# Optimization experiments

Hardware: AMD Instinct MI355X
Metric: run time of the kernel (lower is better)

Reference implementation:

```python
import jax, jax.numpy as jnp
import numpy as np
from jax import lax

B, CIN, H, W = 2, 512, 64, 64
NCLS = 5
CI = CIN // 4      # inter_channels = 128
CQ = CI // 8       # PAM query/key channels = 16
EPS = 1e-5


def setup_inputs() -> dict:
    key = jax.random.key(0)
    it = iter(jax.random.split(key, 48))

    def nrm(shape, s=0.05):
        return jax.random.normal(next(it), shape, jnp.float32) * s

    def bn(c):
        w = jax.random.uniform(next(it), (c,), jnp.float32, 0.5, 1.5)
        b = nrm((c,))
        m = nrm((c,))
        v = jax.random.uniform(next(it), (c,), jnp.float32, 0.5, 1.5)
        return w, b, m, v

    inp = {}
    inp['x'] = jax.random.normal(next(it), (B, CIN, H, W), jnp.float32)
    inp['bn_a_w'], inp['bn_a_b'], inp['bn_a_m'], inp['bn_a_v'] = bn(CIN)
    inp['conv_a_w'] = nrm((CI, CIN, 3, 3))
    inp['bn_c_w'], inp['bn_c_b'], inp['bn_c_m'], inp['bn_c_v'] = bn(CIN)
    inp['conv_c_w'] = nrm((CI, CIN, 3, 3))
    inp['pam_q_w'] = nrm((CQ, CI)); inp['pam_q_b'] = nrm((CQ,))
    inp['pam_k_w'] = nrm((CQ, CI)); inp['pam_k_b'] = nrm((CQ,))
    inp['pam_v_w'] = nrm((CI, CI)); inp['pam_v_b'] = nrm((CI,))
    inp['pam_gamma'] = nrm((1,), 0.5)
    inp['cam_gamma'] = nrm((1,), 0.5)
    inp['bn_a1_w'], inp['bn_a1_b'], inp['bn_a1_m'], inp['bn_a1_v'] = bn(CI)
    inp['conv_a1_w'] = nrm((CIN, CI)); inp['conv_a1_b'] = nrm((CIN,))
    inp['bn_c1_w'], inp['bn_c1_b'], inp['bn_c1_m'], inp['bn_c1_v'] = bn(CI)
    inp['conv_c1_w'] = nrm((CIN, CI)); inp['conv_c1_b'] = nrm((CIN,))
    inp['out_a_w'] = nrm((NCLS, CIN)); inp['out_a_b'] = nrm((NCLS,))
    inp['out_c_w'] = nrm((NCLS, CIN)); inp['out_c_b'] = nrm((NCLS,))
    inp['out_f_w'] = nrm((NCLS, CIN)); inp['out_f_b'] = nrm((NCLS,))
    return inp


def _bn_relu(x, w, b, m, v):
    # eval-mode BatchNorm2d followed by ReLU
    scale = (w / jnp.sqrt(v + EPS))[None, :, None, None]
    shift = (b - m * w / jnp.sqrt(v + EPS))[None, :, None, None]
    return jax.nn.relu(x * scale + shift)


def _conv3(x, w):
    return lax.conv_general_dilated(x, w, (1, 1), 'SAME',
                                    dimension_numbers=('NCHW', 'OIHW', 'NCHW'))


def _conv1(x, w, b):
    # 1x1 conv as channel matmul
    return jnp.einsum('oi,bihw->bohw', w, x) + b[None, :, None, None]


def _pam(x, wq, bq, wk, bk, wv, bv, gamma):
    Bc, C, Hh, Ww = x.shape
    N = Hh * Ww
    q = _conv1(x, wq, bq).reshape(Bc, -1, N)   # [B,CQ,N]
    k = _conv1(x, wk, bk).reshape(Bc, -1, N)   # [B,CQ,N]
    v = _conv1(x, wv, bv).reshape(Bc, C, N)    # [B,C,N]
    energy = jnp.einsum('bcn,bcm->bnm', q, k)  # [B,N,N]
    attn = jax.nn.softmax(energy, axis=-1)
    out = jnp.einsum('bcm,bnm->bcn', v, attn).reshape(Bc, C, Hh, Ww)
    return gamma * out + x


def _cam(x, gamma):
    Bc, C, Hh, Ww = x.shape
    N = Hh * Ww
    f = x.reshape(Bc, C, N)
    energy = jnp.einsum('bcn,bdn->bcd', f, f)                    # [B,C,C]
    energy_new = jnp.max(energy, -1, keepdims=True) - energy
    attn = jax.nn.softmax(energy_new, axis=-1)
    out = jnp.einsum('bcd,bdn->bcn', attn, f).reshape(Bc, C, Hh, Ww)
    return gamma * out + x


def reference(x, bn_a_w, bn_a_b, bn_a_m, bn_a_v, conv_a_w,
              bn_c_w, bn_c_b, bn_c_m, bn_c_v, conv_c_w,
              pam_q_w, pam_q_b, pam_k_w, pam_k_b, pam_v_w, pam_v_b,
              pam_gamma, cam_gamma,
              bn_a1_w, bn_a1_b, bn_a1_m, bn_a1_v, conv_a1_w, conv_a1_b,
              bn_c1_w, bn_c1_b, bn_c1_m, bn_c1_v, conv_c1_w, conv_c1_b,
              out_a_w, out_a_b, out_c_w, out_c_b, out_f_w, out_f_b):
    # position-attention branch
    sa = _conv3(_bn_relu(x, bn_a_w, bn_a_b, bn_a_m, bn_a_v), conv_a_w)
    sa = _pam(sa, pam_q_w, pam_q_b, pam_k_w, pam_k_b, pam_v_w, pam_v_b, pam_gamma)
    sa = _conv1(_bn_relu(sa, bn_a1_w, bn_a1_b, bn_a1_m, bn_a1_v), conv_a1_w, conv_a1_b)
    # channel-attention branch
    sc = _conv3(_bn_relu(x, bn_c_w, bn_c_b, bn_c_m, bn_c_v), conv_c_w)
    sc = _cam(sc, cam_gamma)
    sc = _conv1(_bn_relu(sc, bn_c1_w, bn_c1_b, bn_c1_m, bn_c1_v), conv_c1_w, conv_c1_b)
    feat_fusion = sa + sc
    # dropout is identity at eval time
    sa_out = _conv1(sa, out_a_w, out_a_b)
    sc_out = _conv1(sc, out_c_w, out_c_b)
    sasc_out = _conv1(feat_fusion, out_f_w, out_f_b)
    return (feat_fusion, sasc_out, sa_out, sc_out)
```

## Files before the change

kernel.cpp:

```cpp
#include <hip/hip_runtime.h>

using u16 = unsigned short;
using short8 = __attribute__((ext_vector_type(8))) short;
using f32x4 = __attribute__((ext_vector_type(4))) float;

struct alignas(8) U16x4 { u16 x, y, z, w; };

__device__ __forceinline__ float bf2f(u16 u) {
  return __uint_as_float(((unsigned int)u) << 16);
}
__device__ __forceinline__ u16 f2bf(float f) {
  unsigned int u = __float_as_uint(f);
  unsigned int r = u + 0x7FFFu + ((u >> 16) & 1u);
  return (u16)(r >> 16);
}

__global__ void k_prep_w(const float* __restrict__ wa, const float* __restrict__ wc,
                         u16* __restrict__ Wb) {
  int idx = blockIdx.x * 256 + threadIdx.x;
  int j = idx & 7;
  int l = (idx >> 3) & 63;
  int ks = (idx >> 9) & 3;
  int rest = idx >> 11;
  int tap = rest % 9;
  int rest2 = rest / 9;
  int chunk = rest2 & 3;
  int mt = (rest2 >> 2) & 7;
  int br = rest2 >> 5;
  int co = mt * 16 + (l & 15);
  int ci = chunk * 128 + ks * 32 + (l >> 4) * 8 + j;
  const float* w = br ? wc : wa;
  Wb[idx] = f2bf(w[co * 4608 + ci * 9 + tap]);
}

__global__ void k_prep_w1(const float* __restrict__ wa, const float* __restrict__ wc,
                          u16* __restrict__ W1b) {
  int idx = blockIdx.x * 256 + threadIdx.x;
  int j = idx & 7;
  int l = (idx >> 3) & 63;
  int ks = (idx >> 9) & 3;
  int cot = (idx >> 11) & 31;
  int br = idx >> 16;
  int co = cot * 16 + (l & 15);
  int ci = ks * 32 + (l >> 4) * 8 + j;
  const float* w = br ? wc : wa;
  W1b[idx] = f2bf(w[co * 128 + ci]);
}

__global__ void k_prep_wqkv(const float* __restrict__ wq, const float* __restrict__ wk,
                            const float* __restrict__ wv, u16* __restrict__ Wq) {
  int idx = blockIdx.x * 256 + threadIdx.x;
  if (idx >= 20480) return;
  int j = idx & 7;
  int l = (idx >> 3) & 63;
  int ks = (idx >> 9) & 3;
  int cot = idx >> 11;
  int co = cot * 16 + (l & 15);
  int ci = ks * 32 + (l >> 4) * 8 + j;
  float w = co < 16 ? wq[co * 128 + ci]
          : (co < 32 ? wk[(co - 16) * 128 + ci] : wv[(co - 32) * 128 + ci]);
  Wq[idx] = f2bf(w);
}

__global__ __launch_bounds__(256) void k_bnrelu2t(const float* __restrict__ x,
    const float* __restrict__ wa, const float* __restrict__ ba,
    const float* __restrict__ ma, const float* __restrict__ va,
    const float* __restrict__ wc, const float* __restrict__ bc,
    const float* __restrict__ mc, const float* __restrict__ vc,
    u16* __restrict__ xa16, u16* __restrict__ xcb16) {
  __shared__ float sA[512], bA[512], sC[512], bC[512];
  __shared__ u16 ta[64 * 136], tc[64 * 136];
  int t = threadIdx.x;
  int h = blockIdx.x, b = blockIdx.y;
  for (int c = t; c < 512; c += 256) {
    float s1 = wa[c] * rsqrtf(va[c] + 1e-5f);
    sA[c] = s1; bA[c] = ba[c] - ma[c] * s1;
    float s2 = wc[c] * rsqrtf(vc[c] + 1e-5f);
    sC[c] = s2; bC[c] = bc[c] - mc[c] * s2;
  }
  __syncthreads();
  const float* xb = x + ((size_t)b << 21) + (h << 6);
  u16* oa = xa16 + ((size_t)b << 21) + ((size_t)h << 15);
  u16* oc = xcb16 + ((size_t)b << 21) + ((size_t)h << 15);
  int w = t & 63, cg = t >> 6;
  for (int c0 = 0; c0 < 512; c0 += 128) {
#pragma unroll
    for (int i = 0; i < 8; ++i) {
      int cl = cg * 4 + i * 16;
      int c = c0 + cl;
      const float* xp = xb + (size_t)c * 4096 + w;
      float v0 = xp[0], v1 = xp[4096], v2 = xp[8192], v3 = xp[12288];
      U16x4 pa, pc;
      pa.x = f2bf(fmaxf(fmaf(v0, sA[c], bA[c]), 0.f));
      pa.y = f2bf(fmaxf(fmaf(v1, sA[c + 1], bA[c + 1]), 0.f));
      pa.z = f2bf(fmaxf(fmaf(v2, sA[c + 2], bA[c + 2]), 0.f));
      pa.w = f2bf(fmaxf(fmaf(v3, sA[c + 3], bA[c + 3]), 0.f));
      pc.x = f2bf(fmaxf(fmaf(v0, sC[c], bC[c]), 0.f));
      pc.y = f2bf(fmaxf(fmaf(v1, sC[c + 1], bC[c + 1]), 0.f));
      pc.z = f2bf(fmaxf(fmaf(v2, sC[c + 2], bC[c + 2]), 0.f));
      pc.w = f2bf(fmaxf(fmaf(v3, sC[c + 3], bC[c + 3]), 0.f));
      *(U16x4*)(ta + w * 136 + cl) = pa;
      *(U16x4*)(tc + w * 136 + cl) = pc;
    }
    __syncthreads();
#pragma unroll
    for (int i = 0; i < 4; ++i) {
      int idx = t + i * 256;
      int ww = idx >> 4, c8 = (idx & 15) << 3;
      *(short8*)(oa + (size_t)ww * 512 + c0 + c8) = *(const short8*)(ta + ww * 136 + c8);
      *(short8*)(oc + (size_t)ww * 512 + c0 + c8) = *(const short8*)(tc + ww * 136 + c8);
    }
    __syncthreads();
  }
}

__global__ __launch_bounds__(256, 2) void k_conv3n(
    const u16* __restrict__ xa16, const u16* __restrict__ xcb16,
    const u16* __restrict__ Wb,
    float* __restrict__ sa0, float* __restrict__ sc0,
    u16* __restrict__ sa_nhwc, u16* __restrict__ sc16h, u16* __restrict__ sc16l) {
  __shared__ u16 xs[3 * 66 * 136];
  int t = threadIdx.x;
  int h = blockIdx.x;
  int z = blockIdx.y; int b = z & 1, br = z >> 1;
  int cosplit = blockIdx.z;
  const u16* xb = (br ? xcb16 : xa16) + ((size_t)b << 21);
  const u16* wb = Wb + (size_t)br * 589824;
  float* out = (br ? sc0 : sa0) + (((size_t)b * 128) << 12) + (h << 6);

  int lane = t & 63, wave = t >> 6;
  int mi = lane & 15, quad = lane >> 4;
  int mt = cosplit * 4 + wave;

  if (t < 96) {
    int dh = t >> 5, side = (t >> 4) & 1, c8 = t & 15;
    short8 z8 = {0, 0, 0, 0, 0, 0, 0, 0};
    *(short8*)(xs + (dh * 66 + side * 65) * 136 + c8 * 8) = z8;
  }

  f32x4 acc[4] = {};

  const u16* wlane = wb + lane * 8;
  const u16* bbase0 = xs + mi * 136 + quad * 8;

  for (int chunk = 0; chunk < 4; ++chunk) {
    int ci0 = chunk << 7;
    __syncthreads();
#pragma unroll
    for (int dh = 0; dh < 3; ++dh) {
      int hh = h + dh - 1;
      bool val = (hh >= 0) && (hh < 64);
      const u16* src = xb + (((size_t)hh << 6) << 9) + ci0;
#pragma unroll
      for (int i = 0; i < 4; ++i) {
        int idx = t + i * 256;
        int w = idx >> 4, c8 = (idx & 15) << 3;
        short8 v = {0, 0, 0, 0, 0, 0, 0, 0};
        if (val) v = *(const short8*)(src + ((size_t)w << 9) + c8);
        *(short8*)(xs + (dh * 66 + 1 + w) * 136 + c8) = v;
      }
    }
    __syncthreads();
    const u16* wchunk = wlane + (size_t)(mt * 4 + chunk) * 18432;
    short8 wreg[2][4];
#pragma unroll
    for (int ks = 0; ks < 4; ++ks)
      wreg[0][ks] = *(const short8*)(wchunk + ks * 512);
#pragma unroll
    for (int tap = 0; tap < 9; ++tap) {
      const int cb = tap & 1;
      if (tap < 8) {
        const u16* wn = wchunk + (tap + 1) * 2048;
#pragma unroll
        for (int ks = 0; ks < 4; ++ks)
          wreg[cb ^ 1][ks] = *(const short8*)(wn + ks * 512);
      }
      const int dh = tap / 3, dw = tap % 3;
      const u16* bp = bbase0 + (dh * 66 + dw) * 136;
#pragma unroll
      for (int ks = 0; ks < 4; ++ks) {
        short8 a = wreg[cb][ks];
#pragma unroll
        for (int nt = 0; nt < 4; ++nt) {
          short8 bf = *(const short8*)(bp + nt * 2176 + ks * 32);
          acc[nt] = __builtin_amdgcn_mfma_f32_16x16x32_bf16(a, bf, acc[nt], 0, 0, 0);
        }
      }
    }
  }
#pragma unroll
  for (int nt = 0; nt < 4; ++nt)
#pragma unroll
    for (int r = 0; r < 4; ++r) {
      int co = mt * 16 + quad * 4 + r;
      out[((size_t)co << 12) + nt * 16 + mi] = acc[nt][r];
    }
  if (br == 0) {
    u16* dstq = sa_nhwc + ((size_t)b << 19) + ((size_t)h << 6) * 128;
#pragma unroll
    for (int nt = 0; nt < 4; ++nt) {
      U16x4 v4;
      v4.x = f2bf(acc[nt][0]); v4.y = f2bf(acc[nt][1]);
      v4.z = f2bf(acc[nt][2]); v4.w = f2bf(acc[nt][3]);
      *(U16x4*)(dstq + (size_t)(nt * 16 + mi) * 128 + mt * 16 + quad * 4) = v4;
    }
  } else {
    u16* dh_ = sc16h + ((size_t)b << 19) + (h << 6);
    u16* dl_ = sc16l + ((size_t)b << 19) + (h << 6);
#pragma unroll
    for (int nt = 0; nt < 4; ++nt)
#pragma unroll
      for (int r = 0; r < 4; ++r) {
        int co = mt * 16 + quad * 4 + r;
        float xv = acc[nt][r];
        u16 hi = f2bf(xv);
        float lo = xv - bf2f(hi);
        size_t o = ((size_t)co << 12) + nt * 16 + mi;
        dh_[o] = hi;
        dl_[o] = f2bf(lo);
      }
  }
}

__global__ __launch_bounds__(256) void k_qkv(
    const u16* __restrict__ sa_nhwc, const u16* __restrict__ Wqkvb,
    const float* __restrict__ bq, const float* __restrict__ bk,
    const float* __restrict__ bv,
    float* __restrict__ qb, float* __restrict__ kbuf, u16* __restrict__ vt16) {
  __shared__ float bs[160];
  int t = threadIdx.x;
  int b = blockIdx.y, n0 = blockIdx.x * 128;
  if (t < 160) bs[t] = t < 16 ? bq[t] : (t < 32 ? bk[t - 16] : bv[t - 32]);
  __syncthreads();
  int lane = t & 63, wave = t >> 6;
  int mi = lane & 15, quad = lane >> 4;
  const u16* xb = sa_nhwc + ((size_t)b << 19) + (size_t)n0 * 128;
  const u16* wb = Wqkvb + lane * 8;
  f32x4 acc[2][10] = {};
  short8 bf[2][4];
#pragma unroll
  for (int ns = 0; ns < 2; ++ns) {
    int n = wave * 32 + ns * 16 + mi;
#pragma unroll
    for (int ks = 0; ks < 4; ++ks)
      bf[ns][ks] = *(const short8*)(xb + (size_t)n * 128 + ks * 32 + quad * 8);
  }
#pragma unroll
  for (int cot = 0; cot < 10; ++cot) {
    short8 a0 = *(const short8*)(wb + (size_t)(cot * 4 + 0) * 512);
    short8 a1 = *(const short8*)(wb + (size_t)(cot * 4 + 1) * 512);
    short8 a2 = *(const short8*)(wb + (size_t)(cot * 4 + 2) * 512);
    short8 a3 = *(const short8*)(wb + (size_t)(cot * 4 + 3) * 512);
#pragma unroll
    for (int ns = 0; ns < 2; ++ns) {
      acc[ns][cot] = __builtin_amdgcn_mfma_f32_16x16x32_bf16(a0, bf[ns][0], acc[ns][cot], 0, 0, 0);
      acc[ns][cot] = __builtin_amdgcn_mfma_f32_16x16x32_bf16(a1, bf[ns][1], acc[ns][cot], 0, 0, 0);
      acc[ns][cot] = __builtin_amdgcn_mfma_f32_16x16x32_bf16(a2, bf[ns][2], acc[ns][cot], 0, 0, 0);
      acc[ns][cot] = __builtin_amdgcn_mfma_f32_16x16x32_bf16(a3, bf[ns][3], acc[ns][cot], 0, 0, 0);
    }
  }
#pragma unroll
  for (int cot = 0; cot < 10; ++cot)
#pragma unroll
    for (int ns = 0; ns < 2; ++ns)
#pragma unroll
      for (int r = 0; r < 4; ++r) {
        int co = cot * 16 + quad * 4 + r;
        int n = n0 + wave * 32 + ns * 16 + mi;
        float v = acc[ns][cot][r] + bs[co];
        if (co < 16) qb[((b * 16 + co) << 12) + n] = v;
        else if (co < 32) kbuf[((b * 16 + co - 16) << 12) + n] = v;
        else vt16[((size_t)(b * 128 + co - 32) << 12) + n] = f2bf(v);
      }
}

__global__ __launch_bounds__(512, 4) void k_pam_pv(const float* __restrict__ qb,
    const float* __restrict__ kb, const u16* __restrict__ vt16,
    float* __restrict__ pvpart, float* __restrict__ pmax, float* __restrict__ psum) {
  constexpr int KSTR = 40;
  constexpr int PSTR = 264;
  __shared__ u16 kst[2][256 * KSTR];
  __shared__ u16 pL[32 * PSTR];
  __shared__ u16 qfh[32 * 16], qfl[32 * 16];
  __shared__ float wmx[8][2][16];
  __shared__ float wsm[8][2][16];
  int t = threadIdx.x;
  int b = blockIdx.y, n0 = blockIdx.x * 32;
  int mbeg = blockIdx.z << 11;
  int lane = t & 63, wave = t >> 6;
  int mi = lane & 15, quad = lane >> 4;
  int c0 = wave * 16;
  {
    int ch = t & 15, nl = t >> 4;
    float qv = qb[((size_t)(b * 16 + ch) << 12) + n0 + nl];
    u16 hi = f2bf(qv);
    qfh[nl * 16 + ch] = hi;
    qfl[nl * 16 + ch] = f2bf(qv - bf2f(hi));
  }
  const float* kpb = kb + ((size_t)b * 16 << 12) + mbeg;
  const u16* vb = vt16 + ((size_t)b * 128 << 12);
  f32x4 acc[2] = {};
  float mr0 = -1e30f, mr1 = -1e30f, ssum0 = 0.f, ssum1 = 0.f;
  int sm = t & 255, shalf = t >> 8;
  {
    short8 hi8, lo8;
#pragma unroll
    for (int j = 0; j < 8; ++j) {
      float v = kpb[((size_t)(shalf * 8 + j) << 12) + sm];
      u16 hi = f2bf(v);
      hi8[j] = (short)hi;
      lo8[j] = (short)f2bf(v - bf2f(hi));
    }
    *(short8*)(kst[0] + sm * KSTR + shalf * 8) = hi8;
    *(short8*)(kst[0] + sm * KSTR + 16 + shalf * 8) = lo8;
  }
  __syncthreads();
  int qoff = (quad & 1) * 8;
  short8 bq1[2], bq2[2];
  bq1[0] = *(const short8*)(qfh + mi * 16 + qoff);
  bq1[1] = *(const short8*)(qfh + (16 + mi) * 16 + qoff);
  bq2[0] = *(const short8*)(qfl + mi * 16 + qoff);
  bq2[1] = *(const short8*)(qfl + (16 + mi) * 16 + qoff);
  int cur = 0;
  for (int it = 0; it < 8; ++it) {
    int m0 = mbeg + (it << 8);
    short8 vreg[8];
#pragma unroll
    for (int ksl = 0; ksl < 8; ++ksl)
      vreg[ksl] = *(const short8*)(vb + ((size_t)(c0 + mi) << 12) + m0 + ksl * 32 + quad * 8);
    float kreg[8];
    if (it < 7) {
#pragma unroll
      for (int j = 0; j < 8; ++j)
        kreg[j] = kpb[((size_t)(shalf * 8 + j) << 12) + ((it + 1) << 8) + sm];
    }
    const u16* ka = kst[cur] + (wave * 32) * KSTR;
    short8 a0 = *(const short8*)(ka + mi * KSTR + quad * 8);
    short8 a1 = *(const short8*)(ka + (16 + mi) * KSTR + quad * 8);
    f32x4 e00 = {}, e01 = {}, e10 = {}, e11 = {};
    e00 = __builtin_amdgcn_mfma_f32_16x16x32_bf16(a0, bq1[0], e00, 0, 0, 0);
    e00 = __builtin_amdgcn_mfma_f32_16x16x32_bf16(a0, bq2[0], e00, 0, 0, 0);
    e01 = __builtin_amdgcn_mfma_f32_16x16x32_bf16(a0, bq1[1], e01, 0, 0, 0);
    e01 = __builtin_amdgcn_mfma_f32_16x16x32_bf16(a0, bq2[1], e01, 0, 0, 0);
    e10 = __builtin_amdgcn_mfma_f32_16x16x32_bf16(a1, bq1[0], e10, 0, 0, 0);
    e10 = __builtin_amdgcn_mfma_f32_16x16x32_bf16(a1, bq2[0], e10, 0, 0, 0);
    e11 = __builtin_amdgcn_mfma_f32_16x16x32_bf16(a1, bq1[1], e11, 0, 0, 0);
    e11 = __builtin_amdgcn_mfma_f32_16x16x32_bf16(a1, bq2[1], e11, 0, 0, 0);
    float lm0 = fmaxf(fmaxf(fmaxf(e00[0], e00[1]), fmaxf(e00[2], e00[3])),
                      fmaxf(fmaxf(e10[0], e10[1]), fmaxf(e10[2], e10[3])));
    float lm1 = fmaxf(fmaxf(fmaxf(e01[0], e01[1]), fmaxf(e01[2], e01[3])),
                      fmaxf(fmaxf(e11[0], e11[1]), fmaxf(e11[2], e11[3])));
    lm0 = fmaxf(lm0, __shfl_xor(lm0, 16)); lm0 = fmaxf(lm0, __shfl_xor(lm0, 32));
    lm1 = fmaxf(lm1, __shfl_xor(lm1, 16)); lm1 = fmaxf(lm1, __shfl_xor(lm1, 32));
    if (quad == 0) { wmx[wave][0][mi] = lm0; wmx[wave][1][mi] = lm1; }
    __syncthreads();
    if (it < 7) {
      short8 hi8, lo8;
#pragma unroll
      for (int j = 0; j < 8; ++j) {
        u16 hi = f2bf(kreg[j]);
        hi8[j] = (short)hi;
        lo8[j] = (short)f2bf(kreg[j] - bf2f(hi));
      }
      *(short8*)(kst[cur ^ 1] + sm * KSTR + shalf * 8) = hi8;
      *(short8*)(kst[cur ^ 1] + sm * KSTR + 16 + shalf * 8) = lo8;
    }
    float cm0 = wmx[0][0][mi], cm1 = wmx[0][1][mi];
#pragma unroll
    for (int w = 1; w < 8; ++w) {
      cm0 = fmaxf(cm0, wmx[w][0][mi]);
      cm1 = fmaxf(cm1, wmx[w][1][mi]);
    }
    float mn0 = fmaxf(mr0, cm0), mn1 = fmaxf(mr1, cm1);
    float rs0 = __expf(mr0 - mn0), rs1 = __expf(mr1 - mn1);
#pragma unroll
    for (int r = 0; r < 4; ++r) { acc[0][r] *= rs0; acc[1][r] *= rs1; }
    float p00[4], p10[4], p01[4], p11[4];
    float ls0 = 0.f, ls1 = 0.f;
#pragma unroll
    for (int j = 0; j < 4; ++j) {
      p00[j] = __expf(e00[j] - mn0); p10[j] = __expf(e10[j] - mn0);
      p01[j] = __expf(e01[j] - mn1); p11[j] = __expf(e11[j] - mn1);
      ls0 += p00[j] + p10[j];
      ls1 += p01[j] + p11[j];
    }
    ssum0 = ssum0 * rs0 + ls0;
    ssum1 = ssum1 * rs1 + ls1;
    mr0 = mn0; mr1 = mn1;
    u16* prow0 = pL + mi * PSTR + wave * 32 + quad * 4;
    u16* prow1 = pL + (16 + mi) * PSTR + wave * 32 + quad * 4;
    U16x4 p;
    p.x = f2bf(p00[0]); p.y = f2bf(p00[1]); p.z = f2bf(p00[2]); p.w = f2bf(p00[3]);
    *(U16x4*)(prow0) = p;
    p.x = f2bf(p10[0]); p.y = f2bf(p10[1]); p.z = f2bf(p10[2]); p.w = f2bf(p10[3]);
    *(U16x4*)(prow0 + 16) = p;
    p.x = f2bf(p01[0]); p.y = f2bf(p01[1]); p.z = f2bf(p01[2]); p.w = f2bf(p01[3]);
    *(U16x4*)(prow1) = p;
    p.x = f2bf(p11[0]); p.y = f2bf(p11[1]); p.z = f2bf(p11[2]); p.w = f2bf(p11[3]);
    *(U16x4*)(prow1 + 16) = p;
    __syncthreads();
#pragma unroll
    for (int ksl = 0; ksl < 8; ++ksl) {
      const u16* pb0 = pL + mi * PSTR + ksl * 32 + quad * 8;
      short8 b0 = *(const short8*)(pb0);
      short8 b1 = *(const short8*)(pb0 + 16 * PSTR);
      acc[0] = __builtin_amdgcn_mfma_f32_16x16x32_bf16(vreg[ksl], b0, acc[0], 0, 0, 0);
      acc[1] = __builtin_amdgcn_mfma_f32_16x16x32_bf16(vreg[ksl], b1, acc[1], 0, 0, 0);
    }
    cur ^= 1;
  }
  ssum0 += __shfl_xor(ssum0, 16); ssum0 += __shfl_xor(ssum0, 32);
  ssum1 += __shfl_xor(ssum1, 16); ssum1 += __shfl_xor(ssum1, 32);
  if (quad == 0) { wsm[wave][0][mi] = ssum0; wsm[wave][1][mi] = ssum1; }
  __syncthreads();
  if (t < 16) {
    float sA = 0.f, sB = 0.f;
#pragma unroll
    for (int w = 0; w < 8; ++w) { sA += wsm[w][0][t]; sB += wsm[w][1][t]; }
    size_t base = ((size_t)(blockIdx.z * 2 + b) << 12) + n0;
    psum[base + t] = sA;
    psum[base + 16 + t] = sB;
    pmax[base + t] = mr0;
    pmax[base + 16 + t] = mr1;
  }
  float* dst = pvpart + (((size_t)(blockIdx.z * 2 + b) * 128) << 12);
#pragma unroll
  for (int nh = 0; nh < 2; ++nh)
#pragma unroll
    for (int r = 0; r < 4; ++r) {
      int c = c0 + quad * 4 + r;
      dst[((size_t)c << 12) + n0 + nh * 16 + mi] = acc[nh][r];
    }
}

__global__ __launch_bounds__(512) void k_cam_energy_m(
    const u16* __restrict__ sc16h, const u16* __restrict__ sc16l,
    float* __restrict__ epart) {
  int t = threadIdx.x;
  int ti = blockIdx.x, kc = blockIdx.y, b = blockIdx.z;
  int lane = t & 63, wave = t >> 6;
  int mi = lane & 15, quad = lane >> 4;
  const u16* fh = sc16h + ((size_t)b << 19);
  const u16* fl = sc16l + ((size_t)b << 19);
  size_t ao = ((size_t)(ti * 16 + mi) << 12) + (kc << 9) + quad * 8;
  size_t bo = ((size_t)(wave * 16 + mi) << 12) + (kc << 9) + quad * 8;
  const u16* ah = fh + ao; const u16* al = fl + ao;
  const u16* bh = fh + bo; const u16* bl = fl + bo;
  f32x4 acc = {};
#pragma unroll
  for (int k = 0; k < 16; ++k) {
    short8 vah = *(const short8*)(ah + k * 32);
    short8 val = *(const short8*)(al + k * 32);
    short8 vbh = *(const short8*)(bh + k * 32);
    short8 vbl = *(const short8*)(bl + k * 32);
    acc = __builtin_amdgcn_mfma_f32_16x16x32_bf16(vah, vbh, acc, 0, 0, 0);
    acc = __builtin_amdgcn_mfma_f32_16x16x32_bf16(vah, vbl, acc, 0, 0, 0);
    acc = __builtin_amdgcn_mfma_f32_16x16x32_bf16(val, vbh, acc, 0, 0, 0);
  }
  float* ep = epart + (((size_t)(kc * 2 + b)) << 14);
#pragma unroll
  for (int r = 0; r < 4; ++r)
    ep[((ti * 16 + quad * 4 + r) << 7) + wave * 16 + mi] = acc[r];
}

__global__ void k_cam_softmax(const float* __restrict__ epart, float* __restrict__ attn) {
  int lane = threadIdx.x;
  int c = blockIdx.x, b = blockIdx.y;
  float e0 = 0.f, e1 = 0.f;
#pragma unroll
  for (int kc = 0; kc < 8; ++kc) {
    const float* ep = epart + (((size_t)(kc * 2 + b)) << 14) + (c << 7);
    e0 += ep[lane];
    e1 += ep[lane + 64];
  }
  float mn = fminf(e0, e1);
#pragma unroll
  for (int off = 32; off >= 1; off >>= 1) mn = fminf(mn, __shfl_xor(mn, off));
  float p0 = __expf(fminf(mn - e0, 0.f)), p1 = __expf(fminf(mn - e1, 0.f));
  float s = p0 + p1;
#pragma unroll
  for (int off = 32; off >= 1; off >>= 1) s += __shfl_xor(s, off);
  float inv = 1.f / s;
  float* a = attn + ((b * 128 + c) << 7);
  a[lane] = p0 * inv;
  a[lane + 64] = p1 * inv;
}

__global__ __launch_bounds__(256) void k_cam_out(const float* __restrict__ f,
    const float* __restrict__ attn, const float* __restrict__ gamma,
    float* __restrict__ sc1) {
  __shared__ float at2[128 * 16];
  int t = threadIdx.x;
  int b = blockIdx.z, c0 = blockIdx.y * 16;
  int n = blockIdx.x * 256 + t;
  for (int idx = t; idx < 2048; idx += 256) {
    int d = idx >> 4, cc = idx & 15;
    at2[idx] = attn[((b * 128 + c0 + cc) << 7) + d];
  }
  __syncthreads();
  float acc[16] = {};
  const float* fb = f + ((size_t)b * 128 << 12) + n;
  for (int d = 0; d < 128; ++d) {
    float fv = fb[d << 12];
    const float* ap = at2 + d * 16;
#pragma unroll
    for (int cc = 0; cc < 16; ++cc) acc[cc] = fmaf(ap[cc], fv, acc[cc]);
  }
  float g = gamma[0];
#pragma unroll
  for (int cc = 0; cc < 16; ++cc) {
    size_t o = ((size_t)(b * 128 + c0 + cc) << 12) + n;
    sc1[o] = fmaf(g, acc[cc], f[o]);
  }
}

__global__ __launch_bounds__(256, 2) void k_bout_m(
    const float* __restrict__ sa0, const float* __restrict__ pvpart,
    const float* __restrict__ pmax, const float* __restrict__ psum,
    const float* __restrict__ gamma,
    const float* __restrict__ sc1,
    const float* __restrict__ wa_, const float* __restrict__ ba_,
    const float* __restrict__ ma_, const float* __restrict__ va_,
    const float* __restrict__ wc_, const float* __restrict__ bc_,
    const float* __restrict__ mc_, const float* __restrict__ vc_,
    const u16* __restrict__ W1b, const float* __restrict__ Ba,
    const float* __restrict__ Bc,
    u16* __restrict__ sa2, u16* __restrict__ sc2) {
  __shared__ u16 xl[32 * 136];
  __shared__ float scl[128], shf[128];
  int t = threadIdx.x;
  int n0 = blockIdx.x * 32;
  int b = blockIdx.y, br = blockIdx.z;
  const float* bw = br ? wc_ : wa_;
  const float* bb = br ? bc_ : ba_;
  const float* bm = br ? mc_ : ma_;
  const float* bvv = br ? vc_ : va_;
  if (t < 128) {
    float s = bw[t] * rsqrtf(bvv[t] + 1e-5f);
    scl[t] = s;
    shf[t] = bb[t] - bm[t] * s;
  }
  __syncthreads();
  {
    int nl = t & 31, cio = t >> 5;
    const float* s0 = (br ? sc1 : sa0) + ((size_t)b * 128 << 12) + n0 + nl;
    const float* p0 = pvpart + ((size_t)b * 128 << 12) + n0 + nl;
    const float* p1 = pvpart + (((size_t)(2 + b) * 128) << 12) + n0 + nl;
    float k0 = 0.f, k1 = 0.f;
    if (!br) {
      int n = n0 + nl;
      float m0 = pmax[((size_t)b << 12) + n];
      float m1 = pmax[((size_t)(2 + b) << 12) + n];
      float sA = psum[((size_t)b << 12) + n];
      float sB = psum[((size_t)(2 + b) << 12) + n];
      float M = fmaxf(m0, m1);
      float w0 = __expf(m0 - M), w1 = __expf(m1 - M);
      float inv = gamma[0] / (w0 * sA + w1 * sB);
      k0 = w0 * inv; k1 = w1 * inv;
    }
#pragma unroll
    for (int half = 0; half < 2; ++half) {
      short8 v;
#pragma unroll
      for (int i = 0; i < 8; ++i) {
        int ci = cio * 16 + half * 8 + i;
        float xv = s0[(size_t)ci << 12];
        if (!br) xv += k0 * p0[(size_t)ci << 12] + k1 * p1[(size_t)ci << 12];
        v[i] = (short)f2bf(fmaxf(fmaf(xv, scl[ci], shf[ci]), 0.f));
      }
      *(short8*)(xl + nl * 136 + cio * 16 + half * 8) = v;
    }
  }
  __syncthreads();
  int lane = t & 63, wave = t >> 6;
  int mi = lane & 15, quad = lane >> 4;
  const u16* wb = W1b + (size_t)br * 65536 + lane * 8;
  f32x4 acc[8][2] = {};
#pragma unroll
  for (int ks = 0; ks < 4; ++ks) {
    short8 b0 = *(const short8*)(xl + mi * 136 + ks * 32 + quad * 8);
    short8 b1 = *(const short8*)(xl + (16 + mi) * 136 + ks * 32 + quad * 8);
#pragma unroll
    for (int ct = 0; ct < 8; ++ct) {
      int cot = wave * 8 + ct;
      short8 a = *(const short8*)(wb + ((size_t)(cot * 4 + ks) << 9));
      acc[ct][0] = __builtin_amdgcn_mfma_f32_16x16x32_bf16(a, b0, acc[ct][0], 0, 0, 0);
      acc[ct][1] = __builtin_amdgcn_mfma_f32_16x16x32_bf16(a, b1, acc[ct][1], 0, 0, 0);
    }
  }
  const float* Bs = br ? Bc : Ba;
  u16* dst = br ? sc2 : sa2;
#pragma unroll
  for (int ct = 0; ct < 8; ++ct)
#pragma unroll
    for (int nh = 0; nh < 2; ++nh)
#pragma unroll
      for (int r = 0; r < 4; ++r) {
        int co = (wave * 8 + ct) * 16 + quad * 4 + r;
        dst[((size_t)(b * 512 + co) << 12) + n0 + nh * 16 + mi] =
            f2bf(acc[ct][nh][r] + Bs[co]);
      }
}

__global__ __launch_bounds__(256) void k_heads2(const u16* __restrict__ sa2,
    const u16* __restrict__ sc2,
    const float* __restrict__ wf, const float* __restrict__ wa, const float* __restrict__ wc,
    const float* __restrict__ bfb, const float* __restrict__ bab,
    const float* __restrict__ bcb,
    float* __restrict__ outFusion, float* __restrict__ outCls) {
  __shared__ float lw[3 * 5 * 512];
  __shared__ float hs[8][15][32];
  int t = threadIdx.x;
  int b = blockIdx.y, n0 = blockIdx.x * 32;
  for (int idx = t; idx < 7680; idx += 256) {
    int arr = idx / 2560, rest = idx - arr * 2560;
    int cls = rest >> 9, co = rest & 511;
    const float* w = arr == 0 ? wf : (arr == 1 ? wa : wc);
    lw[idx] = w[cls * 512 + co];
  }
  __syncthreads();
  int nl = t & 31, ck = t >> 5;
  float acc[15] = {};
  for (int co = ck * 64; co < ck * 64 + 64; ++co) {
    size_t o = ((size_t)(b * 512 + co) << 12) + n0 + nl;
    float a = bf2f(sa2[o]), c = bf2f(sc2[o]);
    float s = a + c;
    outFusion[o] = s;
    const float* lf = lw + co;
#pragma unroll
    for (int cls = 0; cls < 5; ++cls) {
      acc[cls]      = fmaf(lf[cls * 512], s, acc[cls]);
      acc[5 + cls]  = fmaf(lf[2560 + cls * 512], a, acc[5 + cls]);
      acc[10 + cls] = fmaf(lf[5120 + cls * 512], c, acc[10 + cls]);
    }
  }
#pragma unroll
  for (int k = 0; k < 15; ++k) hs[ck][k][nl] = acc[k];
  __syncthreads();
  for (int idx = t; idx < 480; idx += 256) {
    int k = idx >> 5, nl2 = idx & 31;
    float s = 0.f;
#pragma unroll
    for (int c8 = 0; c8 < 8; ++c8) s += hs[c8][k][nl2];
    int arr = k / 5, cls = k - arr * 5;
    float bias = arr == 0 ? bfb[cls] : (arr == 1 ? bab[cls] : bcb[cls]);
    outCls[arr * 40960 + ((b * 5 + cls) << 12) + n0 + nl2] = s + bias;
  }
}

extern "C" void kernel_launch(void* const* d_in, const int* in_sizes, int n_in,
                              void* d_out, int out_size, void* d_ws, size_t ws_size,
                              hipStream_t stream) {
  (void)in_sizes; (void)n_in; (void)out_size; (void)ws_size;
  const float* x      = (const float*)d_in[0];
  const float* bnaw   = (const float*)d_in[1];
  const float* bnab   = (const float*)d_in[2];
  const float* bnam   = (const float*)d_in[3];
  const float* bnav   = (const float*)d_in[4];
  const float* convaw = (const float*)d_in[5];
  const float* bncw   = (const float*)d_in[6];
  const float* bncb   = (const float*)d_in[7];
  const float* bncm   = (const float*)d_in[8];
  const float* bncv   = (const float*)d_in[9];
  const float* convcw = (const float*)d_in[10];
  const float* pqw    = (const float*)d_in[11];
  const float* pqb    = (const float*)d_in[12];
  const float* pkw    = (const float*)d_in[13];
  const float* pkb    = (const float*)d_in[14];
  const float* pvw    = (const float*)d_in[15];
  const float* pvb    = (const float*)d_in[16];
  const float* pgam   = (const float*)d_in[17];
  const float* cgam   = (const float*)d_in[18];
  const float* bna1w  = (const float*)d_in[19];
  const float* bna1b  = (const float*)d_in[20];
  const float* bna1m  = (const float*)d_in[21];
  const float* bna1v  = (const float*)d_in[22];
  const float* conva1w = (const float*)d_in[23];
  const float* conva1b = (const float*)d_in[24];
  const float* bnc1w  = (const float*)d_in[25];
  const float* bnc1b  = (const float*)d_in[26];
  const float* bnc1m  = (const float*)d_in[27];
  const float* bnc1v  = (const float*)d_in[28];
  const float* convc1w = (const float*)d_in[29];
  const float* convc1b = (const float*)d_in[30];
  const float* outaw  = (const float*)d_in[31];
  const float* outab  = (const float*)d_in[32];
  const float* outcw  = (const float*)d_in[33];
  const float* outcb  = (const float*)d_in[34];
  const float* outfw  = (const float*)d_in[35];
  const float* outfb  = (const float*)d_in[36];

  char* wsb = (char*)d_ws;
  size_t off = 0;
  auto take = [&](size_t bytes) -> void* {
    void* p = wsb + off;
    off += (bytes + 255) & ~(size_t)255;
    return p;
  };
  u16*   Wb    = (u16*)take((size_t)2 * 128 * 9 * 512 * 2);
  u16*   W1b   = (u16*)take((size_t)2 * 512 * 128 * 2);
  u16*   Wqkvb = (u16*)take((size_t)160 * 128 * 2);
  u16*   xa16  = (u16*)take((size_t)2 * 512 * 4096 * 2);
  u16*   xcb16 = (u16*)take((size_t)2 * 512 * 4096 * 2);
  float* sa0   = (float*)take((size_t)2 * 128 * 4096 * 4);
  float* sc0   = (float*)take((size_t)2 * 128 * 4096 * 4);
  u16*   sa_nhwc = (u16*)take((size_t)2 * 4096 * 128 * 2);
  u16*   sc16h = (u16*)take((size_t)2 * 128 * 4096 * 2);
  u16*   sc16l = (u16*)take((size_t)2 * 128 * 4096 * 2);
  float* qb    = (float*)take((size_t)2 * 16 * 4096 * 4);
  float* kbuf  = (float*)take((size_t)2 * 16 * 4096 * 4);
  u16*   vt16  = (u16*)take((size_t)2 * 128 * 4096 * 2);
  float* pvpart = (float*)take((size_t)2 * 2 * 128 * 4096 * 4);
  float* pmax  = (float*)take((size_t)2 * 2 * 4096 * 4);
  float* psum  = (float*)take((size_t)2 * 2 * 4096 * 4);
  float* sc1   = (float*)take((size_t)2 * 128 * 4096 * 4);
  float* epart = (float*)take((size_t)8 * 2 * 128 * 128 * 4);
  float* attn  = (float*)take((size_t)2 * 128 * 128 * 4);
  u16*   sa2   = (u16*)take((size_t)2 * 512 * 4096 * 2);
  u16*   sc2   = (u16*)take((size_t)2 * 512 * 4096 * 2);

  float* outF = (float*)d_out;
  float* outCls = outF + (size_t)2 * 512 * 4096;

  k_prep_w<<<4608, 256, 0, stream>>>(convaw, convcw, Wb);
  k_prep_w1<<<512, 256, 0, stream>>>(conva1w, convc1w, W1b);
  k_prep_wqkv<<<80, 256, 0, stream>>>(pqw, pkw, pvw, Wqkvb);
  k_bnrelu2t<<<dim3(64, 2), 256, 0, stream>>>(x, bnaw, bnab, bnam, bnav,
                                              bncw, bncb, bncm, bncv, xa16, xcb16);
  k_conv3n<<<dim3(64, 4, 2), 256, 0, stream>>>(xa16, xcb16, Wb, sa0, sc0,
                                               sa_nhwc, sc16h, sc16l);
  k_qkv<<<dim3(32, 2), 256, 0, stream>>>(sa_nhwc, Wqkvb, pqb, pkb, pvb,
                                         qb, kbuf, vt16);
  k_pam_pv<<<dim3(128, 2, 2), 512, 0, stream>>>(qb, kbuf, vt16, pvpart, pmax, psum);
  k_cam_energy_m<<<dim3(8, 8, 2), 512, 0, stream>>>(sc16h, sc16l, epart);
  k_cam_softmax<<<dim3(128, 2), 64, 0, stream>>>(epart, attn);
  k_cam_out<<<dim3(16, 8, 2), 256, 0, stream>>>(sc0, attn, cgam, sc1);
  k_bout_m<<<dim3(128, 2, 2), 256, 0, stream>>>(sa0, pvpart, pmax, psum, pgam, sc1,
      bna1w, bna1b, bna1m, bna1v, bnc1w, bnc1b, bnc1m, bnc1v,
      W1b, conva1b, convc1b, sa2, sc2);
  k_heads2<<<dim3(128, 2), 256, 0, stream>>>(sa2, sc2, outfw, outaw, outcw,
                                             outfb, outab, outcb, outF, outCls);
}
```

Measured before the change: 312.3 us.

## Store PAM keys as pre-split bf16 hi/lo in position-major layout

The QKV kernel now writes the key projection as bf16 hi/lo pairs in a [b][n][32] layout, in place of fp32 channel-major. The PAM kernel then loads MFMA A-operands for keys straight from global memory into registers, prefetching one iteration ahead. This removes the per-block fp32→bf16 split conversion and the double-buffered LDS staging of keys that every one of the 512 blocks repeated. The cost is more scattered 8-byte stores in k_qkv and uncoalesced-ish 16-byte global loads per lane in the attention loop.

Result: no change. 308.1 us (-1.3%).

```diff
diff --git a/kernel.cpp b/kernel.cpp
--- a/kernel.cpp
+++ b/kernel.cpp
@@ -226,7 +226,7 @@
     const u16* __restrict__ sa_nhwc, const u16* __restrict__ Wqkvb,
     const float* __restrict__ bq, const float* __restrict__ bk,
     const float* __restrict__ bv,
-    float* __restrict__ qb, float* __restrict__ kbuf, u16* __restrict__ vt16) {
+    float* __restrict__ qb, u16* __restrict__ k16t, u16* __restrict__ vt16) {
   __shared__ float bs[160];
   int t = threadIdx.x;
   int b = blockIdx.y, n0 = blockIdx.x * 128;
@@ -262,24 +262,38 @@
 #pragma unroll
   for (int cot = 0; cot < 10; ++cot)
 #pragma unroll
-    for (int ns = 0; ns < 2; ++ns)
-#pragma unroll
-      for (int r = 0; r < 4; ++r) {
-        int co = cot * 16 + quad * 4 + r;
-        int n = n0 + wave * 32 + ns * 16 + mi;
-        float v = acc[ns][cot][r] + bs[co];
-        if (co < 16) qb[((b * 16 + co) << 12) + n] = v;
-        else if (co < 32) kbuf[((b * 16 + co - 16) << 12) + n] = v;
-        else vt16[((size_t)(b * 128 + co - 32) << 12) + n] = f2bf(v);
+    for (int ns = 0; ns < 2; ++ns) {
+      int n = n0 + wave * 32 + ns * 16 + mi;
+      if (cot == 1) {
+        u16 hv[4], lv[4];
+#pragma unroll
+        for (int r = 0; r < 4; ++r) {
+          float v = acc[ns][1][r] + bs[16 + quad * 4 + r];
+          u16 hi = f2bf(v);
+          hv[r] = hi;
+          lv[r] = f2bf(v - bf2f(hi));
+        }
+        u16* kd = k16t + (((size_t)b << 12) + n) * 32;
+        U16x4 h4{hv[0], hv[1], hv[2], hv[3]};
+        U16x4 l4{lv[0], lv[1], lv[2], lv[3]};
+        *(U16x4*)(kd + quad * 4) = h4;
+        *(U16x4*)(kd + 16 + quad * 4) = l4;
+      } else {
+#pragma unroll
+        for (int r = 0; r < 4; ++r) {
+          int co = cot * 16 + quad * 4 + r;
+          float v = acc[ns][cot][r] + bs[co];
+          if (co < 16) qb[((b * 16 + co) << 12) + n] = v;
+          else vt16[((size_t)(b * 128 + co - 32) << 12) + n] = f2bf(v);
+        }
       }
+    }
 }
 
 __global__ __launch_bounds__(512, 4) void k_pam_pv(const float* __restrict__ qb,
-    const float* __restrict__ kb, const u16* __restrict__ vt16,
+    const u16* __restrict__ k16t, const u16* __restrict__ vt16,
     float* __restrict__ pvpart, float* __restrict__ pmax, float* __restrict__ psum) {
-  constexpr int KSTR = 40;
   constexpr int PSTR = 264;
-  __shared__ u16 kst[2][256 * KSTR];
   __shared__ u16 pL[32 * PSTR];
   __shared__ u16 qfh[32 * 16], qfl[32 * 16];
   __shared__ float wmx[8][2][16];
@@ -297,23 +311,10 @@
     qfh[nl * 16 + ch] = hi;
     qfl[nl * 16 + ch] = f2bf(qv - bf2f(hi));
   }
-  const float* kpb = kb + ((size_t)b * 16 << 12) + mbeg;
+  const u16* kp = k16t + (((size_t)b << 12) + mbeg) * 32;
   const u16* vb = vt16 + ((size_t)b * 128 << 12);
   f32x4 acc[2] = {};
   float mr0 = -1e30f, mr1 = -1e30f, ssum0 = 0.f, ssum1 = 0.f;
-  int sm = t & 255, shalf = t >> 8;
-  {
-    short8 hi8, lo8;
-#pragma unroll
-    for (int j = 0; j < 8; ++j) {
-      float v = kpb[((size_t)(shalf * 8 + j) << 12) + sm];
-      u16 hi = f2bf(v);
-      hi8[j] = (short)hi;
-      lo8[j] = (short)f2bf(v - bf2f(hi));
-    }
-    *(short8*)(kst[0] + sm * KSTR + shalf * 8) = hi8;
-    *(short8*)(kst[0] + sm * KSTR + 16 + shalf * 8) = lo8;
-  }
   __syncthreads();
   int qoff = (quad & 1) * 8;
   short8 bq1[2], bq2[2];
@@ -321,31 +322,29 @@
   bq1[1] = *(const short8*)(qfh + (16 + mi) * 16 + qoff);
   bq2[0] = *(const short8*)(qfl + mi * 16 + qoff);
   bq2[1] = *(const short8*)(qfl + (16 + mi) * 16 + qoff);
-  int cur = 0;
+  size_t abase = (size_t)(wave * 32 + mi) * 32 + quad * 8;
+  short8 a0c = *(const short8*)(kp + abase);
+  short8 a1c = *(const short8*)(kp + abase + 512);
   for (int it = 0; it < 8; ++it) {
-    int m0 = mbeg + (it << 8);
+    int m0r = it << 8;
     short8 vreg[8];
 #pragma unroll
     for (int ksl = 0; ksl < 8; ++ksl)
-      vreg[ksl] = *(const short8*)(vb + ((size_t)(c0 + mi) << 12) + m0 + ksl * 32 + quad * 8);
-    float kreg[8];
+      vreg[ksl] = *(const short8*)(vb + ((size_t)(c0 + mi) << 12) + mbeg + m0r + ksl * 32 + quad * 8);
+    short8 a0n, a1n;
     if (it < 7) {
-#pragma unroll
-      for (int j = 0; j < 8; ++j)
-        kreg[j] = kpb[((size_t)(shalf * 8 + j) << 12) + ((it + 1) << 8) + sm];
-    }
-    const u16* ka = kst[cur] + (wave * 32) * KSTR;
-    short8 a0 = *(const short8*)(ka + mi * KSTR + quad * 8);
-    short8 a1 = *(const short8*)(ka + (16 + mi) * KSTR + quad * 8);
+      a0n = *(const short8*)(kp + (size_t)(it + 1) * 8192 + abase);
+      a1n = *(const short8*)(kp + (size_t)(it + 1) * 8192 + abase + 512);
+    }
     f32x4 e00 = {}, e01 = {}, e10 = {}, e11 = {};
-    e00 = __builtin_amdgcn_mfma_f32_16x16x32_bf16(a0, bq1[0], e00, 0, 0, 0);
-    e00 = __builtin_amdgcn_mfma_f32_16x16x32_bf16(a0, bq2[0], e00, 0, 0, 0);
-    e01 = __builtin_amdgcn_mfma_f32_16x16x32_bf16(a0, bq1[1], e01, 0, 0, 0);
-    e01 = __builtin_amdgcn_mfma_f32_16x16x32_bf16(a0, bq2[1], e01, 0, 0, 0);
-    e10 = __builtin_amdgcn_mfma_f32_16x16x32_bf16(a1, bq1[0], e10, 0, 0, 0);
-    e10 = __builtin_amdgcn_mfma_f32_16x16x32_bf16(a1, bq2[0], e10, 0, 0, 0);
-    e11 = __builtin_amdgcn_mfma_f32_16x16x32_bf16(a1, bq1[1], e11, 0, 0, 0);
-    e11 = __builtin_amdgcn_mfma_f32_16x16x32_bf16(a1, bq2[1], e11, 0, 0, 0);
+    e00 = __builtin_amdgcn_mfma_f32_16x16x32_bf16(a0c, bq1[0], e00, 0, 0, 0);
+    e00 = __builtin_amdgcn_mfma_f32_16x16x32_bf16(a0c, bq2[0], e00, 0, 0, 0);
+    e01 = __builtin_amdgcn_mfma_f32_16x16x32_bf16(a0c, bq1[1], e01, 0, 0, 0);
+    e01 = __builtin_amdgcn_mfma_f32_16x16x32_bf16(a0c, bq2[1], e01, 0, 0, 0);
+    e10 = __builtin_amdgcn_mfma_f32_16x16x32_bf16(a1c, bq1[0], e10, 0, 0, 0);
+    e10 = __builtin_amdgcn_mfma_f32_16x16x32_bf16(a1c, bq2[0], e10, 0, 0, 0);
+    e11 = __builtin_amdgcn_mfma_f32_16x16x32_bf16(a1c, bq1[1], e11, 0, 0, 0);
+    e11 = __builtin_amdgcn_mfma_f32_16x16x32_bf16(a1c, bq2[1], e11, 0, 0, 0);
     float lm0 = fmaxf(fmaxf(fmaxf(e00[0], e00[1]), fmaxf(e00[2], e00[3])),
                       fmaxf(fmaxf(e10[0], e10[1]), fmaxf(e10[2], e10[3])));
     float lm1 = fmaxf(fmaxf(fmaxf(e01[0], e01[1]), fmaxf(e01[2], e01[3])),
@@ -354,17 +353,6 @@
     lm1 = fmaxf(lm1, __shfl_xor(lm1, 16)); lm1 = fmaxf(lm1, __shfl_xor(lm1, 32));
     if (quad == 0) { wmx[wave][0][mi] = lm0; wmx[wave][1][mi] = lm1; }
     __syncthreads();
-    if (it < 7) {
-      short8 hi8, lo8;
-#pragma unroll
-      for (int j = 0; j < 8; ++j) {
-        u16 hi = f2bf(kreg[j]);
-        hi8[j] = (short)hi;
-        lo8[j] = (short)f2bf(kreg[j] - bf2f(hi));
-      }
-      *(short8*)(kst[cur ^ 1] + sm * KSTR + shalf * 8) = hi8;
-      *(short8*)(kst[cur ^ 1] + sm * KSTR + 16 + shalf * 8) = lo8;
-    }
     float cm0 = wmx[0][0][mi], cm1 = wmx[0][1][mi];
 #pragma unroll
     for (int w = 1; w < 8; ++w) {
@@ -407,7 +395,7 @@
       acc[0] = __builtin_amdgcn_mfma_f32_16x16x32_bf16(vreg[ksl], b0, acc[0], 0, 0, 0);
       acc[1] = __builtin_amdgcn_mfma_f32_16x16x32_bf16(vreg[ksl], b1, acc[1], 0, 0, 0);
     }
-    cur ^= 1;
+    a0c = a0n; a1c = a1n;
   }
   ssum0 += __shfl_xor(ssum0, 16); ssum0 += __shfl_xor(ssum0, 32);
   ssum1 += __shfl_xor(ssum1, 16); ssum1 += __shfl_xor(ssum1, 32);
@@ -708,7 +696,7 @@
   u16*   sc16h = (u16*)take((size_t)2 * 128 * 4096 * 2);
   u16*   sc16l = (u16*)take((size_t)2 * 128 * 4096 * 2);
   float* qb    = (float*)take((size_t)2 * 16 * 4096 * 4);
-  float* kbuf  = (float*)take((size_t)2 * 16 * 4096 * 4);
+  u16*   k16t  = (u16*)take((size_t)2 * 4096 * 32 * 2);
   u16*   vt16  = (u16*)take((size_t)2 * 128 * 4096 * 2);
   float* pvpart = (float*)take((size_t)2 * 2 * 128 * 4096 * 4);
   float* pmax  = (float*)take((size_t)2 * 2 * 4096 * 4);
@@ -730,8 +718,8 @@
   k_conv3n<<<dim3(64, 4, 2), 256, 0, stream>>>(xa16, xcb16, Wb, sa0, sc0,
                                                sa_nhwc, sc16h, sc16l);
   k_qkv<<<dim3(32, 2), 256, 0, stream>>>(sa_nhwc, Wqkvb, pqb, pkb, pvb,
-                                         qb, kbuf, vt16);
-  k_pam_pv<<<dim3(128, 2, 2), 512, 0, stream>>>(qb, kbuf, vt16, pvpart, pmax, psum);
+                                         qb, k16t, vt16);
+  k_pam_pv<<<dim3(128, 2, 2), 512, 0, stream>>>(qb, k16t, vt16, pvpart, pmax, psum);
   k_cam_energy_m<<<dim3(8, 8, 2), 512, 0, stream>>>(sc16h, sc16l, epart);
   k_cam_softmax<<<dim3(128, 2), 64, 0, stream>>>(epart, attn);
   k_cam_out<<<dim3(16, 8, 2), 256, 0, stream>>>(sc0, attn, cgam, sc1);
```
